# Kernel optimization log

Measured on AMD Instinct MI355X. Metric: run time of the kernel, lower is better.

## Reference

```python
import jax, jax.numpy as jnp
import numpy as np

NUM_USERS = 100000
NUM_ITEMS = 50000
N_NODES = NUM_USERS + NUM_ITEMS
LATENT_DIM = 64
XIJ_DIM = 16
N_LAYERS = 3
NNZ = 6400000
BATCH = 8192


def setup_inputs() -> dict:
    key = jax.random.key(0)
    ks = jax.random.split(key, 12)
    return {
        "emb_user": jax.random.normal(ks[0], (NUM_USERS, LATENT_DIM), jnp.float32),
        "emb_item": jax.random.normal(ks[1], (NUM_ITEMS, LATENT_DIM), jnp.float32),
        "emb_user_xij": jax.random.normal(ks[2], (NUM_USERS, XIJ_DIM), jnp.float32),
        "emb_item_xij1": jax.random.normal(ks[3], (NUM_ITEMS, XIJ_DIM), jnp.float32),
        "emb_item_xij0": jax.random.normal(ks[4], (NUM_ITEMS, XIJ_DIM), jnp.float32),
        "w_user": jax.random.normal(ks[5], (1,), jnp.float32),
        "w_item": jax.random.normal(ks[6], (1,), jnp.float32),
        "graph_vals": jax.random.uniform(ks[7], (NNZ,), jnp.float32),
        "graph_rows": jax.random.randint(ks[8], (NNZ,), 0, N_NODES, jnp.int64).astype(jnp.int32),
        "graph_cols": jax.random.randint(ks[9], (NNZ,), 0, N_NODES, jnp.int64).astype(jnp.int32),
        "users": jax.random.randint(ks[10], (BATCH,), 0, NUM_USERS, jnp.int64).astype(jnp.int32),
        "items": jax.random.randint(ks[11], (BATCH,), 0, NUM_ITEMS, jnp.int64).astype(jnp.int32),
        "xij": jax.random.randint(jax.random.fold_in(key, 99), (BATCH,), 0, 2, jnp.int32),
    }


def _spmm(rows, cols, vals, x):
    # y[r] = sum_{e: rows[e]==r} vals[e] * x[cols[e]]
    return jax.ops.segment_sum(vals[:, None] * x[cols], rows, num_segments=N_NODES)


def reference(emb_user, emb_item, emb_user_xij, emb_item_xij1, emb_item_xij0,
              w_user, w_item, graph_vals, graph_rows, graph_cols,
              users, items, xij):
    # LightGCN propagation with running-mean accumulator (fuses the stack+mean)
    all_emb = jnp.concatenate([emb_user, emb_item], axis=0)  # [N, D]
    acc = all_emb
    for _ in range(N_LAYERS):
        all_emb = _spmm(graph_rows, graph_cols, graph_vals, all_emb)
        acc = acc + all_emb
    light_out = acc / (N_LAYERS + 1)
    all_users = light_out[:NUM_USERS]
    all_items = light_out[NUM_USERS:]

    users_emb = w_user * all_users[users]          # [B, D]
    items_emb = w_item * all_items[items]          # [B, D]
    xij_user_emb = emb_user_xij[users]             # [B, Dx]
    xij_item_emb = jnp.where(xij[:, None].astype(bool),
                             emb_item_xij1[items], emb_item_xij0[items])

    users_mix = jax.nn.softmax(jnp.concatenate([users_emb, xij_user_emb], axis=1), axis=1)
    items_mix = jax.nn.sigmoid(jnp.concatenate([items_emb, xij_item_emb], axis=1))
    gamma = jnp.sum(users_mix * items_mix, axis=1)  # [B]
    return gamma
```

## Files before the change

### kernel.cpp

```cpp
#include <hip/hip_runtime.h>
#include <hip/hip_bf16.h>
#include <hip/hip_fp16.h>
#include <math.h>

#define NUM_USERS 100000
#define NUM_ITEMS 50000
#define N_NODES   150000
#define DIM       64
#define VAL_SCALE 16383.0f
#define VAL_INV   (1.0f / 16383.0f)

#define SSHIFT 9
#define SROWS  512
#define NBS    ((N_NODES + SROWS - 1) / SROWS)
#define CAP    16
#define FLUSH  8
#define SCAT_WGS 1280
#define GPAD   16
#define SLOTS  32768
#define PKSLOTS 22744
#define SENTINEL 0xFFFFFFFFu

__global__ void copy_init_kernel(const float4* __restrict__ eu, const float4* __restrict__ ei,
                                 ushort4* __restrict__ cur, int total4) {
    int i = blockIdx.x * blockDim.x + threadIdx.x;
    if (i >= total4) return;
    const int user_lim = NUM_USERS * (DIM / 4);
    float4 v = (i < user_lim) ? eu[i] : ei[i - user_lim];
    ushort4 h;
    h.x = __half_as_ushort(__float2half_rn(v.x));
    h.y = __half_as_ushort(__float2half_rn(v.y));
    h.z = __half_as_ushort(__float2half_rn(v.z));
    h.w = __half_as_ushort(__float2half_rn(v.w));
    cur[i] = h;
}

__global__ void gcur_init_kernel(int* __restrict__ gcur) {
    int b = blockIdx.x * blockDim.x + threadIdx.x;
    if (b < NBS) gcur[b * GPAD] = b * SLOTS;
}

__global__ __launch_bounds__(256) void binned_scatter_kernel(
        const int* __restrict__ rows, const int* __restrict__ cols,
        const float* __restrict__ vals, int* __restrict__ gcur,
        uint2* __restrict__ pk8, int nnz) {
    __shared__ unsigned       lbufA[NBS * CAP];
    __shared__ unsigned short lbufB[NBS * CAP];
    __shared__ int            lcur[NBS];
    int t = threadIdx.x;
    for (int i = t; i < NBS; i += 256) lcur[i] = 0;
    __syncthreads();

    int per_wg = (nnz + gridDim.x - 1) / gridDim.x;
    int e0 = blockIdx.x * per_wg;
    int e1 = min(e0 + per_wg, nnz);

    for (int base = e0; base < e1; base += 512) {
        #pragma unroll
        for (int k = 0; k < 2; ++k) {
            int e = base + k * 256 + t;
            if (e < e1) {
                int r = rows[e];
                unsigned q = __float2uint_rn(vals[e] * VAL_SCALE);
                unsigned ax = (unsigned)cols[e] | (q << 18);
                int b = r >> SSHIFT;
                int pos = atomicAdd(&lcur[b], 1);
                if (pos < CAP) {
                    lbufA[b * CAP + pos] = ax;
                    lbufB[b * CAP + pos] = (unsigned short)(r - (b << SSHIFT));
                } else {
                    atomicSub(&lcur[b], 1);
                    int p = atomicAdd(&gcur[b * GPAD], 8);
                    pk8[p] = make_uint2(ax, (unsigned)r);
                    #pragma unroll
                    for (int j = 1; j < 8; ++j) pk8[p + j] = make_uint2(0u, SENTINEL);
                }
            }
        }
        __syncthreads();
        for (int b2 = t; b2 < NBS; b2 += 256) {
            int c = lcur[b2];
            if (c >= FLUSH) {
                int ng = c >> 3;
                int p = atomicAdd(&gcur[b2 * GPAD], ng * 8);
                unsigned rbase = (unsigned)(b2 << SSHIFT);
                for (int j = 0; j < ng * 8; ++j)
                    pk8[p + j] = make_uint2(lbufA[b2 * CAP + j], rbase + lbufB[b2 * CAP + j]);
                int rem = c - ng * 8;
                for (int j = 0; j < rem; ++j) {
                    lbufA[b2 * CAP + j] = lbufA[b2 * CAP + ng * 8 + j];
                    lbufB[b2 * CAP + j] = lbufB[b2 * CAP + ng * 8 + j];
                }
                lcur[b2] = rem;
            }
        }
        __syncthreads();
    }
    for (int b2 = t; b2 < NBS; b2 += 256) {
        int c = lcur[b2];
        if (c > 0) {
            int p = atomicAdd(&gcur[b2 * GPAD], 8);
            unsigned rbase = (unsigned)(b2 << SSHIFT);
            for (int j = 0; j < c; ++j)
                pk8[p + j] = make_uint2(lbufA[b2 * CAP + j], rbase + lbufB[b2 * CAP + j]);
            for (int j = c; j < 8; ++j) pk8[p + j] = make_uint2(0u, SENTINEL);
        }
    }
}

__global__ __launch_bounds__(256) void bucket_build_kernel(const int* __restrict__ gcur,
                                                           const uint2* __restrict__ pk8,
                                                           unsigned* __restrict__ pk,
                                                           int* __restrict__ rowbeg,
                                                           int* __restrict__ rowend) {
    __shared__ int lc[SROWS];
    __shared__ int ps[256];
    int b  = blockIdx.x;
    int r0 = b * SROWS;
    int nr = min(r0 + SROWS, N_NODES) - r0;
    int t  = threadIdx.x;
    lc[t] = 0; lc[t + 256] = 0;
    __syncthreads();
    int s0 = b * SLOTS;
    int s1 = gcur[b * GPAD];
    for (int i = s0 + t; i < s1; i += 256) {
        uint2 en = pk8[i];
        if (en.y != SENTINEL) atomicAdd(&lc[(int)en.y - r0], 1);
    }
    __syncthreads();
    int c0 = lc[2 * t], c1 = lc[2 * t + 1];
    int pair = c0 + c1;
    ps[t] = pair;
    __syncthreads();
    #pragma unroll
    for (int off = 1; off < 256; off <<= 1) {
        int u = (t >= off) ? ps[t - off] : 0;
        __syncthreads();
        ps[t] += u;
        __syncthreads();
    }
    int base = b * PKSLOTS + ps[t] - pair;
    if (2 * t < nr)     { rowbeg[r0 + 2 * t]     = base;      rowend[r0 + 2 * t]     = base + c0; }
    if (2 * t + 1 < nr) { rowbeg[r0 + 2 * t + 1] = base + c0; rowend[r0 + 2 * t + 1] = base + c0 + c1; }
    lc[2 * t] = base;
    lc[2 * t + 1] = base + c0;
    __syncthreads();
    for (int i = s0 + t; i < s1; i += 256) {
        uint2 en = pk8[i];
        if (en.y != SENTINEL) {
            int p = atomicAdd(&lc[(int)en.y - r0], 1);
            pk[p] = en.x;
        }
    }
}

__global__ __launch_bounds__(256) void pull_kernel(const int* __restrict__ rowbeg,
                                                   const int* __restrict__ rowend,
                                                   const unsigned* __restrict__ pk,
                                                   const __half* __restrict__ x,
                                                   __half* __restrict__ y) {
    int lane = threadIdx.x & 63;
    int wv   = __builtin_amdgcn_readfirstlane(threadIdx.x >> 6);
    int row  = blockIdx.x * 4 + wv;
    if (row >= N_NODES) return;
    int s0 = rowbeg[row];
    int s1 = rowend[row];
    float acc = 0.f;
    int e = s0;
    for (; e + 8 <= s1; e += 8) {
        unsigned p0 = pk[e + 0], p1 = pk[e + 1], p2 = pk[e + 2], p3 = pk[e + 3];
        unsigned p4 = pk[e + 4], p5 = pk[e + 5], p6 = pk[e + 6], p7 = pk[e + 7];
        float x0 = __half2float(x[((p0 & 0x3FFFFu) << 6) + lane]);
        float x1 = __half2float(x[((p1 & 0x3FFFFu) << 6) + lane]);
        float x2 = __half2float(x[((p2 & 0x3FFFFu) << 6) + lane]);
        float x3 = __half2float(x[((p3 & 0x3FFFFu) << 6) + lane]);
        float x4 = __half2float(x[((p4 & 0x3FFFFu) << 6) + lane]);
        float x5 = __half2float(x[((p5 & 0x3FFFFu) << 6) + lane]);
        float x6 = __half2float(x[((p6 & 0x3FFFFu) << 6) + lane]);
        float x7 = __half2float(x[((p7 & 0x3FFFFu) << 6) + lane]);
        acc = fmaf((float)(p0 >> 18), x0, acc);
        acc = fmaf((float)(p1 >> 18), x1, acc);
        acc = fmaf((float)(p2 >> 18), x2, acc);
        acc = fmaf((float)(p3 >> 18), x3, acc);
        acc = fmaf((float)(p4 >> 18), x4, acc);
        acc = fmaf((float)(p5 >> 18), x5, acc);
        acc = fmaf((float)(p6 >> 18), x6, acc);
        acc = fmaf((float)(p7 >> 18), x7, acc);
    }
    for (; e < s1; ++e) {
        unsigned p = pk[e];
        acc = fmaf((float)(p >> 18), __half2float(x[((p & 0x3FFFFu) << 6) + lane]), acc);
    }
    y[((size_t)row << 6) + lane] = __float2half_rn(acc * VAL_INV);
}

__global__ __launch_bounds__(256) void pull_batch_kernel(const int* __restrict__ rowbeg,
                                                         const int* __restrict__ rowend,
                                                         const unsigned* __restrict__ pk,
                                                         const __half* __restrict__ x,
                                                         const int* __restrict__ users,
                                                         const int* __restrict__ items,
                                                         float* __restrict__ acc_c, int batch) {
    int lane = threadIdx.x & 63;
    int wv   = blockIdx.x * 4 + __builtin_amdgcn_readfirstlane(threadIdx.x >> 6);
    if (wv >= 2 * batch) return;
    int row = (wv < batch) ? users[wv] : NUM_USERS + items[wv - batch];
    int s0 = rowbeg[row];
    int s1 = rowend[row];
    float acc = 0.f;
    int e = s0;
    for (; e + 8 <= s1; e += 8) {
        unsigned p0 = pk[e + 0], p1 = pk[e + 1], p2 = pk[e + 2], p3 = pk[e + 3];
        unsigned p4 = pk[e + 4], p5 = pk[e + 5], p6 = pk[e + 6], p7 = pk[e + 7];
        float x0 = __half2float(x[((p0 & 0x3FFFFu) << 6) + lane]);
        float x1 = __half2float(x[((p1 & 0x3FFFFu) << 6) + lane]);
        float x2 = __half2float(x[((p2 & 0x3FFFFu) << 6) + lane]);
        float x3 = __half2float(x[((p3 & 0x3FFFFu) << 6) + lane]);
        float x4 = __half2float(x[((p4 & 0x3FFFFu) << 6) + lane]);
        float x5 = __half2float(x[((p5 & 0x3FFFFu) << 6) + lane]);
        float x6 = __half2float(x[((p6 & 0x3FFFFu) << 6) + lane]);
        float x7 = __half2float(x[((p7 & 0x3FFFFu) << 6) + lane]);
        acc = fmaf((float)(p0 >> 18), x0, acc);
        acc = fmaf((float)(p1 >> 18), x1, acc);
        acc = fmaf((float)(p2 >> 18), x2, acc);
        acc = fmaf((float)(p3 >> 18), x3, acc);
        acc = fmaf((float)(p4 >> 18), x4, acc);
        acc = fmaf((float)(p5 >> 18), x5, acc);
        acc = fmaf((float)(p6 >> 18), x6, acc);
        acc = fmaf((float)(p7 >> 18), x7, acc);
    }
    for (; e < s1; ++e) {
        unsigned p = pk[e];
        acc = fmaf((float)(p >> 18), __half2float(x[((p & 0x3FFFFu) << 6) + lane]), acc);
    }
    acc_c[((size_t)wv << 6) + lane] += acc * VAL_INV;
}

__global__ void acc_init_kernel(const float* __restrict__ eu, const float* __restrict__ ei,
                                const int* __restrict__ users, const int* __restrict__ items,
                                float* __restrict__ acc_c, int batch) {
    int gid = blockIdx.x * blockDim.x + threadIdx.x;
    int j = gid >> 6, lane = gid & 63;
    if (j >= 2 * batch) return;
    int row = (j < batch) ? users[j] : NUM_USERS + items[j - batch];
    float v = (row < NUM_USERS) ? eu[((size_t)row << 6) + lane]
                                : ei[((size_t)(row - NUM_USERS) << 6) + lane];
    acc_c[((size_t)j << 6) + lane] = v;
}

__global__ void acc_add_kernel(const __half* __restrict__ y, const int* __restrict__ users,
                               const int* __restrict__ items, float* __restrict__ acc_c,
                               int batch) {
    int gid = blockIdx.x * blockDim.x + threadIdx.x;
    int j = gid >> 6, lane = gid & 63;
    if (j >= 2 * batch) return;
    int row = (j < batch) ? users[j] : NUM_USERS + items[j - batch];
    acc_c[((size_t)j << 6) + lane] += __half2float(y[((size_t)row << 6) + lane]);
}

__global__ void final_kernel(const float* __restrict__ acc_c,
                             const float* __restrict__ exu,
                             const float* __restrict__ exi1,
                             const float* __restrict__ exi0,
                             const float* __restrict__ w_user,
                             const float* __restrict__ w_item,
                             const int* __restrict__ users,
                             const int* __restrict__ items,
                             const int* __restrict__ xijf,
                             float* __restrict__ out, int batch) {
    int gid = blockIdx.x * blockDim.x + threadIdx.x;
    int wave = gid >> 6;
    int lane = threadIdx.x & 63;
    if (wave >= batch) return;

    int u  = users[wave];
    int it = items[wave];
    int xf = xijf[wave];
    float wu = w_user[0] * 0.25f;
    float wi = w_item[0] * 0.25f;

    float ua = wu * acc_c[((size_t)wave << 6) + lane];
    float ia = wi * acc_c[((size_t)(batch + wave) << 6) + lane];
    float ub = -INFINITY, ib = 0.f;
    if (lane < 16) {
        ub = exu[(size_t)u * 16 + lane];
        ib = xf ? exi1[(size_t)it * 16 + lane] : exi0[(size_t)it * 16 + lane];
    }

    float m = fmaxf(ua, ub);
    #pragma unroll
    for (int off = 32; off; off >>= 1) m = fmaxf(m, __shfl_xor(m, off));
    float ea = expf(ua - m);
    float eb = (lane < 16) ? expf(ub - m) : 0.f;
    float s = ea + eb;
    #pragma unroll
    for (int off = 32; off; off >>= 1) s += __shfl_xor(s, off);
    float inv = 1.f / s;

    float sa = 1.f / (1.f + expf(-ia));
    float sb = (lane < 16) ? 1.f / (1.f + expf(-ib)) : 0.f;

    float g = ea * inv * sa + eb * inv * sb;
    #pragma unroll
    for (int off = 32; off; off >>= 1) g += __shfl_xor(g, off);
    if (lane == 0) out[wave] = g;
}

extern "C" void kernel_launch(void* const* d_in, const int* in_sizes, int n_in,
                              void* d_out, int out_size, void* d_ws, size_t ws_size,
                              hipStream_t stream) {
    const float* emb_user = (const float*)d_in[0];
    const float* emb_item = (const float*)d_in[1];
    const float* exu      = (const float*)d_in[2];
    const float* exi1     = (const float*)d_in[3];
    const float* exi0     = (const float*)d_in[4];
    const float* w_user   = (const float*)d_in[5];
    const float* w_item   = (const float*)d_in[6];
    const float* gvals    = (const float*)d_in[7];
    const int*   grows    = (const int*)d_in[8];
    const int*   gcols    = (const int*)d_in[9];
    const int*   users    = (const int*)d_in[10];
    const int*   items    = (const int*)d_in[11];
    const int*   xijf     = (const int*)d_in[12];
    float*       out      = (float*)d_out;

    const int nnz   = in_sizes[7];
    const int batch = in_sizes[10];

    const size_t node_elems = (size_t)N_NODES * DIM;
    const size_t PK8_BYTES  = (size_t)NBS * SLOTS * 8;
    char* w = (char*)d_ws;
    uint2*    pk8   = (uint2*)w;
    __half*   cur   = (__half*)w;
    __half*   nxt   = cur + node_elems;
    float*    acc_c = (float*)(w + 2 * node_elems * sizeof(__half));
    w += PK8_BYTES;
    unsigned* pk     = (unsigned*)w;              w += (size_t)NBS * PKSLOTS * 4;
    int*      rowbeg = (int*)w;                   w += (size_t)N_NODES * 4;
    int*      rowend = (int*)w;                   w += (size_t)N_NODES * 4;
    int*      gcur   = (int*)w;                   w += (size_t)NBS * GPAD * 4;

    const int tb = 256;
    const int total4 = N_NODES * (DIM / 4);

    gcur_init_kernel<<<(NBS + tb - 1) / tb, tb, 0, stream>>>(gcur);
    binned_scatter_kernel<<<SCAT_WGS, 256, 0, stream>>>(grows, gcols, gvals, gcur, pk8, nnz);
    bucket_build_kernel<<<NBS, 256, 0, stream>>>(gcur, pk8, pk, rowbeg, rowend);

    copy_init_kernel<<<(total4 + tb - 1) / tb, tb, 0, stream>>>(
        (const float4*)emb_user, (const float4*)emb_item, (ushort4*)cur, total4);
    acc_init_kernel<<<(2 * batch * DIM + tb - 1) / tb, tb, 0, stream>>>(
        emb_user, emb_item, users, items, acc_c, batch);

    const int pull_blocks = (N_NODES + 3) / 4;
    const int pb_blocks   = (2 * batch + 3) / 4;
    const int accb = (2 * batch * DIM + tb - 1) / tb;

    pull_kernel<<<pull_blocks, tb, 0, stream>>>(rowbeg, rowend, pk, cur, nxt);
    acc_add_kernel<<<accb, tb, 0, stream>>>(nxt, users, items, acc_c, batch);
    pull_kernel<<<pull_blocks, tb, 0, stream>>>(rowbeg, rowend, pk, nxt, cur);
    acc_add_kernel<<<accb, tb, 0, stream>>>(cur, users, items, acc_c, batch);
    pull_batch_kernel<<<pb_blocks, tb, 0, stream>>>(
        rowbeg, rowend, pk, cur, users, items, acc_c, batch);

    final_kernel<<<(batch * 64 + tb - 1) / tb, tb, 0, stream>>>(
        acc_c, exu, exi1, exi0, w_user, w_item, users, items, xijf, out, batch);
}
```

Before: 590.3 us.

## Fuse batch tail into one kernel, vectorize scatter/bucket passes, unroll pull wider

The per-batch accumulation kernels (acc_init, two acc_add, pull_batch, final) are replaced by a single tail kernel. It recomputes the layer-3 rows only for batch users and items, and sums the fp32 input with the fp16 layer-1 and layer-2 buffers directly. The binned scatter now loads rows, cols and vals as int2/float2 pairs and writes packed entries with uint4 stores. Bucket build uses 512 threads with one row per thread and uint4 reads unrolled four deep. The row gather loop gains a 16-way unrolled path to raise memory-level parallelism, at the cost of more registers and some code duplication.

```diff
diff --git a/kernel.cpp b/kernel.cpp
--- a/kernel.cpp
+++ b/kernel.cpp
@@ -20,6 +20,7 @@
 #define SLOTS  32768
 #define PKSLOTS 22744
 #define SENTINEL 0xFFFFFFFFu
+#define BBT 512
 
 __global__ void copy_init_kernel(const float4* __restrict__ eu, const float4* __restrict__ ei,
                                  ushort4* __restrict__ cur, int total4) {
@@ -51,18 +52,21 @@
     for (int i = t; i < NBS; i += 256) lcur[i] = 0;
     __syncthreads();
 
-    int per_wg = (nnz + gridDim.x - 1) / gridDim.x;
+    int per_wg = (((nnz + (int)gridDim.x - 1) / (int)gridDim.x) + 1) & ~1;
     int e0 = blockIdx.x * per_wg;
     int e1 = min(e0 + per_wg, nnz);
 
     for (int base = e0; base < e1; base += 512) {
-        #pragma unroll
-        for (int k = 0; k < 2; ++k) {
-            int e = base + k * 256 + t;
-            if (e < e1) {
-                int r = rows[e];
-                unsigned q = __float2uint_rn(vals[e] * VAL_SCALE);
-                unsigned ax = (unsigned)cols[e] | (q << 18);
+        int e = base + t * 2;
+        if (e + 1 < e1) {
+            int2   r2 = *(const int2*)(rows + e);
+            int2   c2 = *(const int2*)(cols + e);
+            float2 v2 = *(const float2*)(vals + e);
+            #pragma unroll
+            for (int k = 0; k < 2; ++k) {
+                int r = k ? r2.y : r2.x;
+                unsigned q = __float2uint_rn((k ? v2.y : v2.x) * VAL_SCALE);
+                unsigned ax = (unsigned)(k ? c2.y : c2.x) | (q << 18);
                 int b = r >> SSHIFT;
                 int pos = atomicAdd(&lcur[b], 1);
                 if (pos < CAP) {
@@ -71,10 +75,28 @@
                 } else {
                     atomicSub(&lcur[b], 1);
                     int p = atomicAdd(&gcur[b * GPAD], 8);
-                    pk8[p] = make_uint2(ax, (unsigned)r);
-                    #pragma unroll
-                    for (int j = 1; j < 8; ++j) pk8[p + j] = make_uint2(0u, SENTINEL);
+                    *(uint4*)(&pk8[p])     = make_uint4(ax, (unsigned)r, 0u, SENTINEL);
+                    *(uint4*)(&pk8[p + 2]) = make_uint4(0u, SENTINEL, 0u, SENTINEL);
+                    *(uint4*)(&pk8[p + 4]) = make_uint4(0u, SENTINEL, 0u, SENTINEL);
+                    *(uint4*)(&pk8[p + 6]) = make_uint4(0u, SENTINEL, 0u, SENTINEL);
                 }
+            }
+        } else if (e < e1) {
+            int r = rows[e];
+            unsigned q = __float2uint_rn(vals[e] * VAL_SCALE);
+            unsigned ax = (unsigned)cols[e] | (q << 18);
+            int b = r >> SSHIFT;
+            int pos = atomicAdd(&lcur[b], 1);
+            if (pos < CAP) {
+                lbufA[b * CAP + pos] = ax;
+                lbufB[b * CAP + pos] = (unsigned short)(r - (b << SSHIFT));
+            } else {
+                atomicSub(&lcur[b], 1);
+                int p = atomicAdd(&gcur[b * GPAD], 8);
+                *(uint4*)(&pk8[p])     = make_uint4(ax, (unsigned)r, 0u, SENTINEL);
+                *(uint4*)(&pk8[p + 2]) = make_uint4(0u, SENTINEL, 0u, SENTINEL);
+                *(uint4*)(&pk8[p + 4]) = make_uint4(0u, SENTINEL, 0u, SENTINEL);
+                *(uint4*)(&pk8[p + 6]) = make_uint4(0u, SENTINEL, 0u, SENTINEL);
             }
         }
         __syncthreads();
@@ -84,8 +106,11 @@
                 int ng = c >> 3;
                 int p = atomicAdd(&gcur[b2 * GPAD], ng * 8);
                 unsigned rbase = (unsigned)(b2 << SSHIFT);
-                for (int j = 0; j < ng * 8; ++j)
-                    pk8[p + j] = make_uint2(lbufA[b2 * CAP + j], rbase + lbufB[b2 * CAP + j]);
+                for (int j = 0; j < ng * 8; j += 2) {
+                    uint4 q = make_uint4(lbufA[b2 * CAP + j],     rbase + lbufB[b2 * CAP + j],
+                                         lbufA[b2 * CAP + j + 1], rbase + lbufB[b2 * CAP + j + 1]);
+                    *(uint4*)(&pk8[p + j]) = q;
+                }
                 int rem = c - ng * 8;
                 for (int j = 0; j < rem; ++j) {
                     lbufA[b2 * CAP + j] = lbufA[b2 * CAP + ng * 8 + j];
@@ -101,72 +126,121 @@
         if (c > 0) {
             int p = atomicAdd(&gcur[b2 * GPAD], 8);
             unsigned rbase = (unsigned)(b2 << SSHIFT);
-            for (int j = 0; j < c; ++j)
-                pk8[p + j] = make_uint2(lbufA[b2 * CAP + j], rbase + lbufB[b2 * CAP + j]);
-            for (int j = c; j < 8; ++j) pk8[p + j] = make_uint2(0u, SENTINEL);
+            for (int j = 0; j < 8; j += 2) {
+                unsigned a0 = (j     < c) ? lbufA[b2 * CAP + j]     : 0u;
+                unsigned b0 = (j     < c) ? rbase + lbufB[b2 * CAP + j]     : SENTINEL;
+                unsigned a1 = (j + 1 < c) ? lbufA[b2 * CAP + j + 1] : 0u;
+                unsigned b1 = (j + 1 < c) ? rbase + lbufB[b2 * CAP + j + 1] : SENTINEL;
+                *(uint4*)(&pk8[p + j]) = make_uint4(a0, b0, a1, b1);
+            }
         }
     }
 }
 
-__global__ __launch_bounds__(256) void bucket_build_kernel(const int* __restrict__ gcur,
+__global__ __launch_bounds__(BBT) void bucket_build_kernel(const int* __restrict__ gcur,
                                                            const uint2* __restrict__ pk8,
                                                            unsigned* __restrict__ pk,
                                                            int* __restrict__ rowbeg,
                                                            int* __restrict__ rowend) {
     __shared__ int lc[SROWS];
-    __shared__ int ps[256];
+    __shared__ int ps[SROWS];
     int b  = blockIdx.x;
     int r0 = b * SROWS;
     int nr = min(r0 + SROWS, N_NODES) - r0;
     int t  = threadIdx.x;
-    lc[t] = 0; lc[t + 256] = 0;
+    lc[t] = 0;
     __syncthreads();
-    int s0 = b * SLOTS;
-    int s1 = gcur[b * GPAD];
-    for (int i = s0 + t; i < s1; i += 256) {
-        uint2 en = pk8[i];
-        if (en.y != SENTINEL) atomicAdd(&lc[(int)en.y - r0], 1);
-    }
+
+    const uint4* p4 = (const uint4*)pk8;
+    int i0   = (b * SLOTS) >> 1;
+    int iend = gcur[b * GPAD] >> 1;
+
+    #define CNT(q) { \
+        if ((q).y != SENTINEL) atomicAdd(&lc[(int)(q).y - r0], 1); \
+        if ((q).w != SENTINEL) atomicAdd(&lc[(int)(q).w - r0], 1); }
+
+    int i = i0 + t;
+    for (; i + 3 * BBT < iend; i += 4 * BBT) {
+        uint4 qa = p4[i], qb = p4[i + BBT], qc = p4[i + 2 * BBT], qd = p4[i + 3 * BBT];
+        CNT(qa) CNT(qb) CNT(qc) CNT(qd)
+    }
+    for (; i < iend; i += BBT) { uint4 qa = p4[i]; CNT(qa) }
     __syncthreads();
-    int c0 = lc[2 * t], c1 = lc[2 * t + 1];
-    int pair = c0 + c1;
-    ps[t] = pair;
+
+    int c = lc[t];
+    ps[t] = c;
     __syncthreads();
     #pragma unroll
-    for (int off = 1; off < 256; off <<= 1) {
+    for (int off = 1; off < SROWS; off <<= 1) {
         int u = (t >= off) ? ps[t - off] : 0;
         __syncthreads();
         ps[t] += u;
         __syncthreads();
     }
-    int base = b * PKSLOTS + ps[t] - pair;
-    if (2 * t < nr)     { rowbeg[r0 + 2 * t]     = base;      rowend[r0 + 2 * t]     = base + c0; }
-    if (2 * t + 1 < nr) { rowbeg[r0 + 2 * t + 1] = base + c0; rowend[r0 + 2 * t + 1] = base + c0 + c1; }
-    lc[2 * t] = base;
-    lc[2 * t + 1] = base + c0;
+    int base = b * PKSLOTS + ps[t] - c;
+    if (t < nr) { rowbeg[r0 + t] = base; rowend[r0 + t] = base + c; }
+    lc[t] = base;
     __syncthreads();
-    for (int i = s0 + t; i < s1; i += 256) {
-        uint2 en = pk8[i];
-        if (en.y != SENTINEL) {
-            int p = atomicAdd(&lc[(int)en.y - r0], 1);
-            pk[p] = en.x;
-        }
-    }
-}
-
-__global__ __launch_bounds__(256) void pull_kernel(const int* __restrict__ rowbeg,
-                                                   const int* __restrict__ rowend,
-                                                   const unsigned* __restrict__ pk,
-                                                   const __half* __restrict__ x,
-                                                   __half* __restrict__ y) {
-    int lane = threadIdx.x & 63;
-    int wv   = __builtin_amdgcn_readfirstlane(threadIdx.x >> 6);
-    int row  = blockIdx.x * 4 + wv;
-    if (row >= N_NODES) return;
+
+    #define PLC(q) { \
+        if ((q).y != SENTINEL) { int p_ = atomicAdd(&lc[(int)(q).y - r0], 1); pk[p_] = (q).x; } \
+        if ((q).w != SENTINEL) { int p_ = atomicAdd(&lc[(int)(q).w - r0], 1); pk[p_] = (q).z; } }
+
+    i = i0 + t;
+    for (; i + 3 * BBT < iend; i += 4 * BBT) {
+        uint4 qa = p4[i], qb = p4[i + BBT], qc = p4[i + 2 * BBT], qd = p4[i + 3 * BBT];
+        PLC(qa) PLC(qb) PLC(qc) PLC(qd)
+    }
+    for (; i < iend; i += BBT) { uint4 qa = p4[i]; PLC(qa) }
+}
+
+__device__ __forceinline__ float row_pull(const int* __restrict__ rowbeg,
+                                          const int* __restrict__ rowend,
+                                          const unsigned* __restrict__ pk,
+                                          const __half* __restrict__ x,
+                                          int row, int lane) {
     int s0 = rowbeg[row];
     int s1 = rowend[row];
     float acc = 0.f;
     int e = s0;
+    for (; e + 16 <= s1; e += 16) {
+        unsigned p0 = pk[e + 0],  p1 = pk[e + 1],  p2 = pk[e + 2],  p3 = pk[e + 3];
+        unsigned p4 = pk[e + 4],  p5 = pk[e + 5],  p6 = pk[e + 6],  p7 = pk[e + 7];
+        unsigned p8 = pk[e + 8],  p9 = pk[e + 9],  pA = pk[e + 10], pB = pk[e + 11];
+        unsigned pC = pk[e + 12], pD = pk[e + 13], pE = pk[e + 14], pF = pk[e + 15];
+        float x0 = __half2float(x[((p0 & 0x3FFFFu) << 6) + lane]);
+        float x1 = __half2float(x[((p1 & 0x3FFFFu) << 6) + lane]);
+        float x2 = __half2float(x[((p2 & 0x3FFFFu) << 6) + lane]);
+        float x3 = __half2float(x[((p3 & 0x3FFFFu) << 6) + lane]);
+        float x4 = __half2float(x[((p4 & 0x3FFFFu) << 6) + lane]);
+        float x5 = __half2float(x[((p5 & 0x3FFFFu) << 6) + lane]);
+        float x6 = __half2float(x[((p6 & 0x3FFFFu) << 6) + lane]);
+        float x7 = __half2float(x[((p7 & 0x3FFFFu) << 6) + lane]);
+        float x8 = __half2float(x[((p8 & 0x3FFFFu) << 6) + lane]);
+        float x9 = __half2float(x[((p9 & 0x3FFFFu) << 6) + lane]);
+        float xA = __half2float(x[((pA & 0x3FFFFu) << 6) + lane]);
+        float xB = __half2float(x[((pB & 0x3FFFFu) << 6) + lane]);
+        float xC = __half2float(x[((pC & 0x3FFFFu) << 6) + lane]);
+        float xD = __half2float(x[((pD & 0x3FFFFu) << 6) + lane]);
+        float xE = __half2float(x[((pE & 0x3FFFFu) << 6) + lane]);
+        float xF = __half2float(x[((pF & 0x3FFFFu) << 6) + lane]);
+        acc = fmaf((float)(p0 >> 18), x0, acc);
+        acc = fmaf((float)(p1 >> 18), x1, acc);
+        acc = fmaf((float)(p2 >> 18), x2, acc);
+        acc = fmaf((float)(p3 >> 18), x3, acc);
+        acc = fmaf((float)(p4 >> 18), x4, acc);
+        acc = fmaf((float)(p5 >> 18), x5, acc);
+        acc = fmaf((float)(p6 >> 18), x6, acc);
+        acc = fmaf((float)(p7 >> 18), x7, acc);
+        acc = fmaf((float)(p8 >> 18), x8, acc);
+        acc = fmaf((float)(p9 >> 18), x9, acc);
+        acc = fmaf((float)(pA >> 18), xA, acc);
+        acc = fmaf((float)(pB >> 18), xB, acc);
+        acc = fmaf((float)(pC >> 18), xC, acc);
+        acc = fmaf((float)(pD >> 18), xD, acc);
+        acc = fmaf((float)(pE >> 18), xE, acc);
+        acc = fmaf((float)(pF >> 18), xF, acc);
+    }
     for (; e + 8 <= s1; e += 8) {
         unsigned p0 = pk[e + 0], p1 = pk[e + 1], p2 = pk[e + 2], p3 = pk[e + 3];
         unsigned p4 = pk[e + 4], p5 = pk[e + 5], p6 = pk[e + 6], p7 = pk[e + 7];
@@ -191,96 +265,64 @@
         unsigned p = pk[e];
         acc = fmaf((float)(p >> 18), __half2float(x[((p & 0x3FFFFu) << 6) + lane]), acc);
     }
-    y[((size_t)row << 6) + lane] = __float2half_rn(acc * VAL_INV);
-}
-
-__global__ __launch_bounds__(256) void pull_batch_kernel(const int* __restrict__ rowbeg,
-                                                         const int* __restrict__ rowend,
-                                                         const unsigned* __restrict__ pk,
-                                                         const __half* __restrict__ x,
-                                                         const int* __restrict__ users,
-                                                         const int* __restrict__ items,
-                                                         float* __restrict__ acc_c, int batch) {
+    return acc * VAL_INV;
+}
+
+__global__ __launch_bounds__(256) void pull_kernel(const int* __restrict__ rowbeg,
+                                                   const int* __restrict__ rowend,
+                                                   const unsigned* __restrict__ pk,
+                                                   const __half* __restrict__ x,
+                                                   __half* __restrict__ y) {
+    int lane = threadIdx.x & 63;
+    int wv   = __builtin_amdgcn_readfirstlane(threadIdx.x >> 6);
+    int row  = blockIdx.x * 4 + wv;
+    if (row >= N_NODES) return;
+    float acc = row_pull(rowbeg, rowend, pk, x, row, lane);
+    y[((size_t)row << 6) + lane] = __float2half_rn(acc);
+}
+
+__global__ __launch_bounds__(256) void tail_kernel(const int* __restrict__ rowbeg,
+                                                   const int* __restrict__ rowend,
+                                                   const unsigned* __restrict__ pk,
+                                                   const __half* __restrict__ cur,
+                                                   const __half* __restrict__ nxt,
+                                                   const float* __restrict__ eu,
+                                                   const float* __restrict__ ei,
+                                                   const float* __restrict__ exu,
+                                                   const float* __restrict__ exi1,
+                                                   const float* __restrict__ exi0,
+                                                   const float* __restrict__ w_user,
+                                                   const float* __restrict__ w_item,
+                                                   const int* __restrict__ users,
+                                                   const int* __restrict__ items,
+                                                   const int* __restrict__ xijf,
+                                                   float* __restrict__ out, int batch) {
     int lane = threadIdx.x & 63;
     int wv   = blockIdx.x * 4 + __builtin_amdgcn_readfirstlane(threadIdx.x >> 6);
-    if (wv >= 2 * batch) return;
-    int row = (wv < batch) ? users[wv] : NUM_USERS + items[wv - batch];
-    int s0 = rowbeg[row];
-    int s1 = rowend[row];
-    float acc = 0.f;
-    int e = s0;
-    for (; e + 8 <= s1; e += 8) {
-        unsigned p0 = pk[e + 0], p1 = pk[e + 1], p2 = pk[e + 2], p3 = pk[e + 3];
-        unsigned p4 = pk[e + 4], p5 = pk[e + 5], p6 = pk[e + 6], p7 = pk[e + 7];
-        float x0 = __half2float(x[((p0 & 0x3FFFFu) << 6) + lane]);
-        float x1 = __half2float(x[((p1 & 0x3FFFFu) << 6) + lane]);
-        float x2 = __half2float(x[((p2 & 0x3FFFFu) << 6) + lane]);
-        float x3 = __half2float(x[((p3 & 0x3FFFFu) << 6) + lane]);
-        float x4 = __half2float(x[((p4 & 0x3FFFFu) << 6) + lane]);
-        float x5 = __half2float(x[((p5 & 0x3FFFFu) << 6) + lane]);
-        float x6 = __half2float(x[((p6 & 0x3FFFFu) << 6) + lane]);
-        float x7 = __half2float(x[((p7 & 0x3FFFFu) << 6) + lane]);
-        acc = fmaf((float)(p0 >> 18), x0, acc);
-        acc = fmaf((float)(p1 >> 18), x1, acc);
-        acc = fmaf((float)(p2 >> 18), x2, acc);
-        acc = fmaf((float)(p3 >> 18), x3, acc);
-        acc = fmaf((float)(p4 >> 18), x4, acc);
-        acc = fmaf((float)(p5 >> 18), x5, acc);
-        acc = fmaf((float)(p6 >> 18), x6, acc);
-        acc = fmaf((float)(p7 >> 18), x7, acc);
-    }
-    for (; e < s1; ++e) {
-        unsigned p = pk[e];
-        acc = fmaf((float)(p >> 18), __half2float(x[((p & 0x3FFFFu) << 6) + lane]), acc);
-    }
-    acc_c[((size_t)wv << 6) + lane] += acc * VAL_INV;
-}
-
-__global__ void acc_init_kernel(const float* __restrict__ eu, const float* __restrict__ ei,
-                                const int* __restrict__ users, const int* __restrict__ items,
-                                float* __restrict__ acc_c, int batch) {
-    int gid = blockIdx.x * blockDim.x + threadIdx.x;
-    int j = gid >> 6, lane = gid & 63;
-    if (j >= 2 * batch) return;
-    int row = (j < batch) ? users[j] : NUM_USERS + items[j - batch];
-    float v = (row < NUM_USERS) ? eu[((size_t)row << 6) + lane]
-                                : ei[((size_t)(row - NUM_USERS) << 6) + lane];
-    acc_c[((size_t)j << 6) + lane] = v;
-}
-
-__global__ void acc_add_kernel(const __half* __restrict__ y, const int* __restrict__ users,
-                               const int* __restrict__ items, float* __restrict__ acc_c,
-                               int batch) {
-    int gid = blockIdx.x * blockDim.x + threadIdx.x;
-    int j = gid >> 6, lane = gid & 63;
-    if (j >= 2 * batch) return;
-    int row = (j < batch) ? users[j] : NUM_USERS + items[j - batch];
-    acc_c[((size_t)j << 6) + lane] += __half2float(y[((size_t)row << 6) + lane]);
-}
-
-__global__ void final_kernel(const float* __restrict__ acc_c,
-                             const float* __restrict__ exu,
-                             const float* __restrict__ exi1,
-                             const float* __restrict__ exi0,
-                             const float* __restrict__ w_user,
-                             const float* __restrict__ w_item,
-                             const int* __restrict__ users,
-                             const int* __restrict__ items,
-                             const int* __restrict__ xijf,
-                             float* __restrict__ out, int batch) {
-    int gid = blockIdx.x * blockDim.x + threadIdx.x;
-    int wave = gid >> 6;
-    int lane = threadIdx.x & 63;
-    if (wave >= batch) return;
-
-    int u  = users[wave];
-    int it = items[wave];
-    int xf = xijf[wave];
+    if (wv >= batch) return;
+    int u    = users[wv];
+    int it   = items[wv];
+    int xf   = xijf[wv];
+    int rowU = u;
+    int rowI = NUM_USERS + it;
+
+    float l3u = row_pull(rowbeg, rowend, pk, cur, rowU, lane);
+    float l3i = row_pull(rowbeg, rowend, pk, cur, rowI, lane);
+
     float wu = w_user[0] * 0.25f;
     float wi = w_item[0] * 0.25f;
 
-    float ua = wu * acc_c[((size_t)wave << 6) + lane];
-    float ia = wi * acc_c[((size_t)(batch + wave) << 6) + lane];
+    float su = eu[((size_t)u  << 6) + lane]
+             + __half2float(nxt[((size_t)rowU << 6) + lane])
+             + __half2float(cur[((size_t)rowU << 6) + lane])
+             + l3u;
+    float si = ei[((size_t)it << 6) + lane]
+             + __half2float(nxt[((size_t)rowI << 6) + lane])
+             + __half2float(cur[((size_t)rowI << 6) + lane])
+             + l3i;
+    float ua = wu * su;
+    float ia = wi * si;
+
     float ub = -INFINITY, ib = 0.f;
     if (lane < 16) {
         ub = exu[(size_t)u * 16 + lane];
@@ -303,7 +345,7 @@
     float g = ea * inv * sa + eb * inv * sb;
     #pragma unroll
     for (int off = 32; off; off >>= 1) g += __shfl_xor(g, off);
-    if (lane == 0) out[wave] = g;
+    if (lane == 0) out[wv] = g;
 }
 
 extern "C" void kernel_launch(void* const* d_in, const int* in_sizes, int n_in,
@@ -333,7 +375,6 @@
     uint2*    pk8   = (uint2*)w;
     __half*   cur   = (__half*)w;
     __half*   nxt   = cur + node_elems;
-    float*    acc_c = (float*)(w + 2 * node_elems * sizeof(__half));
     w += PK8_BYTES;
     unsigned* pk     = (unsigned*)w;              w += (size_t)NBS * PKSLOTS * 4;
     int*      rowbeg = (int*)w;                   w += (size_t)N_NODES * 4;
@@ -345,24 +386,17 @@
 
     gcur_init_kernel<<<(NBS + tb - 1) / tb, tb, 0, stream>>>(gcur);
     binned_scatter_kernel<<<SCAT_WGS, 256, 0, stream>>>(grows, gcols, gvals, gcur, pk8, nnz);
-    bucket_build_kernel<<<NBS, 256, 0, stream>>>(gcur, pk8, pk, rowbeg, rowend);
+    bucket_build_kernel<<<NBS, BBT, 0, stream>>>(gcur, pk8, pk, rowbeg, rowend);
 
     copy_init_kernel<<<(total4 + tb - 1) / tb, tb, 0, stream>>>(
         (const float4*)emb_user, (const float4*)emb_item, (ushort4*)cur, total4);
-    acc_init_kernel<<<(2 * batch * DIM + tb - 1) / tb, tb, 0, stream>>>(
-        emb_user, emb_item, users, items, acc_c, batch);
 
     const int pull_blocks = (N_NODES + 3) / 4;
-    const int pb_blocks   = (2 * batch + 3) / 4;
-    const int accb = (2 * batch * DIM + tb - 1) / tb;
+    const int tail_blocks = (batch + 3) / 4;
 
     pull_kernel<<<pull_blocks, tb, 0, stream>>>(rowbeg, rowend, pk, cur, nxt);
-    acc_add_kernel<<<accb, tb, 0, stream>>>(nxt, users, items, acc_c, batch);
     pull_kernel<<<pull_blocks, tb, 0, stream>>>(rowbeg, rowend, pk, nxt, cur);
-    acc_add_kernel<<<accb, tb, 0, stream>>>(cur, users, items, acc_c, batch);
-    pull_batch_kernel<<<pb_blocks, tb, 0, stream>>>(
-        rowbeg, rowend, pk, cur, users, items, acc_c, batch);
-
-    final_kernel<<<(batch * 64 + tb - 1) / tb, tb, 0, stream>>>(
-        acc_c, exu, exi1, exi0, w_user, w_item, users, items, xijf, out, batch);
-}
+    tail_kernel<<<tail_blocks, tb, 0, stream>>>(
+        rowbeg, rowend, pk, cur, nxt, emb_user, emb_item,
+        exu, exi1, exi0, w_user, w_item, users, items, xijf, out, batch);
+}
```

Measured after the change: 519.3 us. 12.0% less time.
